# Optimization experiments

Measured on AMD Instinct MI355X. Metric: run time of the kernel, lower is better.

## Reference

```python
import jax, jax.numpy as jnp
import numpy as np

N_NODES = 50000
N_EDGES = 800000
N_GRAPHS = 512
F_IN = 96
HID = 128


def gcn_conv(x, src, dst, W, b, n_nodes):
    # PyG GCNConv: add self-loops, symmetric normalization, scatter-add aggregation.
    h = x @ W  # [N, H] transform first (cheaper than per-edge transform)
    # in-degree from edges (weight 1) plus the self-loop
    deg = jax.ops.segment_sum(jnp.ones_like(dst, dtype=h.dtype), dst,
                              num_segments=n_nodes) + 1.0  # [N]
    dinv = jax.lax.rsqrt(deg)  # D^{-1/2}
    norm = dinv[src] * dinv[dst]  # [E] edge norm
    msg = h[src] * norm[:, None]  # [E, H] gather + scale
    agg = jax.ops.segment_sum(msg, dst, num_segments=n_nodes)  # scatter-add
    agg = agg + h * (1.0 / deg)[:, None]  # self-loop contribution (norm = 1/deg)
    return agg + b


def global_mean_pool(x, batch, num_graphs):
    sums = jax.ops.segment_sum(x, batch, num_segments=num_graphs)  # [G, H]
    cnt = jax.ops.segment_sum(jnp.ones((x.shape[0],), x.dtype), batch,
                              num_segments=num_graphs)  # [G]
    return sums / jnp.maximum(cnt, 1.0)[:, None]


def setup_inputs() -> dict:
    key = jax.random.key(0)
    ks = jax.random.split(key, 8)
    x = jax.random.normal(ks[0], (N_NODES, F_IN), dtype=jnp.float32)
    edge_index = jax.random.randint(ks[1], (2, N_EDGES), 0, N_NODES, dtype=jnp.int64)
    batch = jnp.sort(jax.random.randint(ks[2], (N_NODES,), 0, N_GRAPHS, dtype=jnp.int64))
    W1 = jax.random.normal(ks[3], (F_IN, HID), dtype=jnp.float32) * (1.0 / np.sqrt(F_IN))
    b1 = jnp.zeros((HID,), jnp.float32)
    W2 = jax.random.normal(ks[4], (HID, HID), dtype=jnp.float32) * (1.0 / np.sqrt(HID))
    b2 = jnp.zeros((HID,), jnp.float32)
    Wlin = jax.random.normal(ks[5], (HID, 2), dtype=jnp.float32) * (1.0 / np.sqrt(HID))
    blin = jnp.zeros((2,), jnp.float32)
    return {"x": x, "edge_index": edge_index, "batch": batch, "num_graphs": N_GRAPHS,
            "W1": W1, "b1": b1, "W2": W2, "b2": b2, "Wlin": Wlin, "blin": blin}


def reference(x, edge_index, batch, num_graphs, W1, b1, W2, b2, Wlin, blin):
    src, dst = edge_index[0], edge_index[1]
    n = x.shape[0]
    h = jax.nn.relu(gcn_conv(x, src, dst, W1, b1, n))
    h = jax.nn.relu(gcn_conv(h, src, dst, W2, b2, n))
    g = global_mean_pool(h, batch, num_graphs)  # [G, H]
    # dropout(p=0.2) is identity in eval mode
    return g @ Wlin + blin  # [G, 2]
```

## Files before the change

### kernel.cpp

```cpp
#include <hip/hip_runtime.h>

#define N_NODES 50000
#define N_PAD   50048
#define N_EDGES 800000
#define N_GRAPHS 512
#define F_IN 96
#define HID 128
#define NBUCK 196
#define CHUNK 4096
#define NCH   196
#define NB_G 782

typedef __bf16 bf16x8 __attribute__((ext_vector_type(8)));
typedef float  f32x4  __attribute__((ext_vector_type(4)));

__device__ __forceinline__ unsigned short f2bf(float f) {
    union { float f; unsigned u; } v; v.f = f;
    unsigned r = v.u + 0x7FFFu + ((v.u >> 16) & 1u);
    return (unsigned short)(r >> 16);
}
__device__ __forceinline__ float bflo(unsigned u) {
    union { unsigned u; float f; } v; v.u = u << 16; return v.f;
}
__device__ __forceinline__ float bfhi(unsigned u) {
    union { unsigned u; float f; } v; v.u = u & 0xFFFF0000u; return v.f;
}

__device__ __forceinline__ uint4 frag_of(const float* __restrict__ W, int KS, int idx) {
    int t = idx / (KS * 64);
    int rem = idx % (KS * 64);
    int s = rem / 64;
    int l = rem & 63;
    int n = t * 16 + (l & 15);
    int k0 = s * 32 + (l >> 4) * 8;
    unsigned short v[8];
#pragma unroll
    for (int j = 0; j < 8; ++j) v[j] = f2bf(W[(long)(k0 + j) * 128 + n]);
    uint4 o;
    o.x = (unsigned)v[0] | ((unsigned)v[1] << 16);
    o.y = (unsigned)v[2] | ((unsigned)v[3] << 16);
    o.z = (unsigned)v[4] | ((unsigned)v[5] << 16);
    o.w = (unsigned)v[6] | ((unsigned)v[7] << 16);
    return o;
}

__global__ __launch_bounds__(256) void k1_fused(const int* __restrict__ dst,
                                                const float* __restrict__ W1,
                                                const float* __restrict__ W2,
                                                unsigned short* __restrict__ W2f,
                                                int* __restrict__ bh,
                                                const float* __restrict__ x,
                                                unsigned short* __restrict__ hp) {
    __shared__ uint4 w1lds[1536];
    int blk = blockIdx.x;
    int tid = threadIdx.x;

    if (blk < NB_G) {
        for (int idx = tid; idx < 1536; idx += 256) w1lds[idx] = frag_of(W1, 3, idx);
        __syncthreads();

        const int KS = 3;
        const int wave = tid >> 6, lane = tid & 63;
        const int r0 = blk * 64 + wave * 16;
        f32x4 acc[8];
#pragma unroll
        for (int t = 0; t < 8; ++t) acc[t] = (f32x4){0.f, 0.f, 0.f, 0.f};
        int arow = r0 + (lane & 15);
        if (arow >= N_NODES) arow = N_NODES - 1;
        const int kq = (lane >> 4) * 8;
        for (int s = 0; s < KS; ++s) {
            const float* ap = x + (long)arow * F_IN + s * 32 + kq;
            float4 a0 = *(const float4*)(ap);
            float4 a1 = *(const float4*)(ap + 4);
            union { uint4 u; bf16x8 b; } af;
            af.u.x = (unsigned)f2bf(a0.x) | ((unsigned)f2bf(a0.y) << 16);
            af.u.y = (unsigned)f2bf(a0.z) | ((unsigned)f2bf(a0.w) << 16);
            af.u.z = (unsigned)f2bf(a1.x) | ((unsigned)f2bf(a1.y) << 16);
            af.u.w = (unsigned)f2bf(a1.z) | ((unsigned)f2bf(a1.w) << 16);
#pragma unroll
            for (int t = 0; t < 8; ++t) {
                union { uint4 u; bf16x8 b; } bfr;
                bfr.u = w1lds[(t * KS + s) * 64 + lane];
                acc[t] = __builtin_amdgcn_mfma_f32_16x16x32_bf16(af.b, bfr.b, acc[t], 0, 0, 0);
            }
        }
        const int q = lane >> 4;
#pragma unroll
        for (int t = 0; t < 8; ++t) {
            int col = t * 16 + (lane & 15);
#pragma unroll
            for (int r = 0; r < 4; ++r) {
                int row = r0 + q * 4 + r;
                if (row < N_NODES) hp[(long)row * 128 + col] = f2bf(acc[t][r]);
            }
        }
    } else if (blk < NB_G + NCH) {
        int* bhist = (int*)w1lds;
        int c = blk - NB_G;
        for (int i = tid; i < NBUCK; i += 256) bhist[i] = 0;
        __syncthreads();
        int e0 = c * CHUNK, e1 = min(e0 + CHUNK, N_EDGES);
        int n4 = (e1 - e0) >> 2;
        const uint4* d4 = (const uint4*)(dst + e0);
        for (int i = tid; i < n4; i += 256) {
            uint4 d = d4[i];
            atomicAdd(&bhist[d.x >> 8], 1);
            atomicAdd(&bhist[d.y >> 8], 1);
            atomicAdd(&bhist[d.z >> 8], 1);
            atomicAdd(&bhist[d.w >> 8], 1);
        }
        __syncthreads();
        for (int i = tid; i < NBUCK; i += 256) bh[c * NBUCK + i] = bhist[i];
    } else {
        int idx = (blk - NB_G - NCH) * 256 + tid;
        *(uint4*)(W2f + (long)idx * 8) = frag_of(W2, 4, idx);
    }
}

__global__ __launch_bounds__(256) void goff_scan(const int* __restrict__ bh,
                                                 int* __restrict__ goff,
                                                 int* __restrict__ total) {
    __shared__ int s[256];
    int b = blockIdx.x;
    int c = threadIdx.x;
    int v = (c < NCH) ? bh[c * NBUCK + b] : 0;
    s[c] = v;
    __syncthreads();
#pragma unroll
    for (int off = 1; off < 256; off <<= 1) {
        int t = 0;
        if (c >= off) t = s[c - off];
        __syncthreads();
        if (c >= off) s[c] += t;
        __syncthreads();
    }
    if (c < NCH) goff[c * NBUCK + b] = s[c] - v;
    if (c == 255) total[b] = s[255];
}

__global__ __launch_bounds__(256) void scatter_pairs(const int* __restrict__ src,
                                                     const int* __restrict__ dst,
                                                     const int* __restrict__ goff,
                                                     const int* __restrict__ total,
                                                     unsigned* __restrict__ ebuf) {
    __shared__ int ts[256];
    __shared__ int lgoff[NBUCK];
    __shared__ int lcur[NBUCK];
    int tid = threadIdx.x;
    int c = blockIdx.x;
    int tv = (tid < NBUCK) ? total[tid] : 0;
    ts[tid] = tv;
    __syncthreads();
#pragma unroll
    for (int off = 1; off < 256; off <<= 1) {
        int t = 0;
        if (tid >= off) t = ts[tid - off];
        __syncthreads();
        if (tid >= off) ts[tid] += t;
        __syncthreads();
    }
    if (tid < NBUCK) {
        lgoff[tid] = goff[c * NBUCK + tid] + (ts[tid] - tv);
        lcur[tid] = 0;
    }
    __syncthreads();
    int e0 = c * CHUNK, e1 = min(e0 + CHUNK, N_EDGES);
    for (int e = e0 + tid; e < e1; e += 256) {
        int d = dst[e];
        int b = d >> 8;
        int slot = atomicAdd(&lcur[b], 1);
        ebuf[lgoff[b] + slot] = (unsigned)src[e] | ((unsigned)(d & 255) << 16);
    }
}

__global__ __launch_bounds__(256) void bucket_sort(const unsigned* __restrict__ ebuf,
                                                   const int* __restrict__ total,
                                                   int* __restrict__ rowstart,
                                                   int* __restrict__ cnt,
                                                   float* __restrict__ dinv,
                                                   int* __restrict__ esrc) {
    __shared__ int ts[256];
    __shared__ int lcnt[256];
    __shared__ int ssc[256];
    __shared__ int ncur[256];
    int b = blockIdx.x, tid = threadIdx.x;
    int tv = (tid < NBUCK) ? total[tid] : 0;
    ts[tid] = tv;
    __syncthreads();
#pragma unroll
    for (int off = 1; off < 256; off <<= 1) {
        int t = 0;
        if (tid >= off) t = ts[tid - off];
        __syncthreads();
        if (tid >= off) ts[tid] += t;
        __syncthreads();
    }
    int r1 = ts[b];
    int r0 = r1 - total[b];
    int nbase = b * 256;
    lcnt[tid] = 0;
    __syncthreads();
    for (int i = r0 + tid; i < r1; i += 256)
        atomicAdd(&lcnt[ebuf[i] >> 16], 1);
    __syncthreads();
    int c = lcnt[tid];
    ssc[tid] = c;
    __syncthreads();
#pragma unroll
    for (int off = 1; off < 256; off <<= 1) {
        int t = 0;
        if (tid >= off) t = ssc[tid - off];
        __syncthreads();
        if (tid >= off) ssc[tid] += t;
        __syncthreads();
    }
    int rs = r0 + ssc[tid] - c;
    ncur[tid] = rs;
    int node = nbase + tid;
    if (node < N_NODES) {
        rowstart[node] = rs;
        cnt[node] = c;
        dinv[node] = rsqrtf((float)c + 1.0f);
    }
    __syncthreads();
    for (int i = r0 + tid; i < r1; i += 256) {
        unsigned p = ebuf[i];
        int pos = atomicAdd(&ncur[p >> 16], 1);
        esrc[pos] = (int)(p & 0xFFFFu);
    }
}

__global__ __launch_bounds__(256) void aggregate_w(const uint4* __restrict__ hp4,
                                                   const int* __restrict__ esrc,
                                                   const int* __restrict__ rowstart,
                                                   const int* __restrict__ cnt,
                                                   const float* __restrict__ dinv,
                                                   const float* __restrict__ bias,
                                                   uint4* __restrict__ hout4) {
    int node = blockIdx.x * 4 + (threadIdx.x >> 6);
    if (node >= N_NODES) return;
    int lane = threadIdx.x & 63;
    int eslot = lane >> 4;
    int ug = lane & 15;
    int start = rowstart[node];
    int end = start + cnt[node];

    float a[8];
#pragma unroll
    for (int k = 0; k < 8; ++k) a[k] = 0.f;

    for (int j = start; j < end; j += 16) {
        int e[4];
        uint4 v[4];
        float w[4];
#pragma unroll
        for (int q = 0; q < 4; ++q) {
            e[q] = j + q * 4 + eslot;
            int s = esrc[min(e[q], end - 1)];
            v[q] = hp4[(long)s * 16 + ug];
            w[q] = dinv[s];
        }
#pragma unroll
        for (int q = 0; q < 4; ++q) {
            if (e[q] < end) {
                a[0] += w[q] * bflo(v[q].x); a[1] += w[q] * bfhi(v[q].x);
                a[2] += w[q] * bflo(v[q].y); a[3] += w[q] * bfhi(v[q].y);
                a[4] += w[q] * bflo(v[q].z); a[5] += w[q] * bfhi(v[q].z);
                a[6] += w[q] * bflo(v[q].w); a[7] += w[q] * bfhi(v[q].w);
            }
        }
    }

#pragma unroll
    for (int k = 0; k < 8; ++k) {
        a[k] += __shfl_xor(a[k], 16);
        a[k] += __shfl_xor(a[k], 32);
    }

    if (eslot == 0) {
        float d = dinv[node];
        uint4 vs = hp4[(long)node * 16 + ug];
        a[0] += d * bflo(vs.x); a[1] += d * bfhi(vs.x);
        a[2] += d * bflo(vs.y); a[3] += d * bfhi(vs.y);
        a[4] += d * bflo(vs.z); a[5] += d * bfhi(vs.z);
        a[6] += d * bflo(vs.w); a[7] += d * bfhi(vs.w);
        float4 b0 = *(const float4*)(bias + ug * 8);
        float4 b1 = *(const float4*)(bias + ug * 8 + 4);
        float o0 = fmaxf(d * a[0] + b0.x, 0.f), o1 = fmaxf(d * a[1] + b0.y, 0.f);
        float o2 = fmaxf(d * a[2] + b0.z, 0.f), o3 = fmaxf(d * a[3] + b0.w, 0.f);
        float o4 = fmaxf(d * a[4] + b1.x, 0.f), o5 = fmaxf(d * a[5] + b1.y, 0.f);
        float o6 = fmaxf(d * a[6] + b1.z, 0.f), o7 = fmaxf(d * a[7] + b1.w, 0.f);
        uint4 o;
        o.x = (unsigned)f2bf(o0) | ((unsigned)f2bf(o1) << 16);
        o.y = (unsigned)f2bf(o2) | ((unsigned)f2bf(o3) << 16);
        o.z = (unsigned)f2bf(o4) | ((unsigned)f2bf(o5) << 16);
        o.w = (unsigned)f2bf(o6) | ((unsigned)f2bf(o7) << 16);
        hout4[(long)node * 16 + ug] = o;
    }
}

__global__ __launch_bounds__(256) void gemm_mfma_bf16A(const unsigned short* __restrict__ A,
                                                       const unsigned short* __restrict__ Wf,
                                                       const float* __restrict__ dinv,
                                                       unsigned short* __restrict__ hp) {
    const int KS = 4;
    const int wave = threadIdx.x >> 6;
    const int lane = threadIdx.x & 63;
    const int r0 = blockIdx.x * 64 + wave * 16;

    f32x4 acc[8];
#pragma unroll
    for (int t = 0; t < 8; ++t) acc[t] = (f32x4){0.f, 0.f, 0.f, 0.f};

    const int arow = r0 + (lane & 15);
    const int kq = (lane >> 4) * 8;

    for (int s = 0; s < KS; ++s) {
        union { uint4 u; bf16x8 b; } af;
        af.u = *(const uint4*)(A + (long)arow * HID + s * 32 + kq);
#pragma unroll
        for (int t = 0; t < 8; ++t) {
            union { uint4 u; bf16x8 b; } bfr;
            bfr.u = *(const uint4*)(Wf + ((long)(t * KS + s) * 64 + lane) * 8);
            acc[t] = __builtin_amdgcn_mfma_f32_16x16x32_bf16(af.b, bfr.b, acc[t], 0, 0, 0);
        }
    }

    const int q = lane >> 4;
    float dv[4];
#pragma unroll
    for (int r = 0; r < 4; ++r) {
        int row = r0 + q * 4 + r;
        dv[r] = dinv[row < N_NODES ? row : 0];
    }
#pragma unroll
    for (int t = 0; t < 8; ++t) {
        int col = t * 16 + (lane & 15);
#pragma unroll
        for (int r = 0; r < 4; ++r) {
            int row = r0 + q * 4 + r;
            if (row < N_NODES)
                hp[(long)row * 128 + col] = f2bf(acc[t][r] * dv[r]);
        }
    }
}

__global__ __launch_bounds__(256) void aggregate4(const uint4* __restrict__ hp4,
                                                  const int* __restrict__ esrc,
                                                  const int* __restrict__ rowstart,
                                                  const int* __restrict__ cnt,
                                                  const float* __restrict__ dinv,
                                                  const float* __restrict__ bias,
                                                  uint4* __restrict__ hout4) {
    int node = blockIdx.x * 4 + (threadIdx.x >> 6);
    if (node >= N_NODES) return;
    int lane = threadIdx.x & 63;
    int eslot = lane >> 4;
    int ug = lane & 15;
    int start = rowstart[node];
    int end = start + cnt[node];

    float a[8];
#pragma unroll
    for (int k = 0; k < 8; ++k) a[k] = 0.f;

    for (int j = start; j < end; j += 16) {
        int e[4];
        uint4 v[4];
#pragma unroll
        for (int q = 0; q < 4; ++q) {
            e[q] = j + q * 4 + eslot;
            int s = esrc[min(e[q], end - 1)];
            v[q] = hp4[(long)s * 16 + ug];
        }
#pragma unroll
        for (int q = 0; q < 4; ++q) {
            if (e[q] < end) {
                a[0] += bflo(v[q].x); a[1] += bfhi(v[q].x);
                a[2] += bflo(v[q].y); a[3] += bfhi(v[q].y);
                a[4] += bflo(v[q].z); a[5] += bfhi(v[q].z);
                a[6] += bflo(v[q].w); a[7] += bfhi(v[q].w);
            }
        }
    }

#pragma unroll
    for (int k = 0; k < 8; ++k) {
        a[k] += __shfl_xor(a[k], 16);
        a[k] += __shfl_xor(a[k], 32);
    }

    if (eslot == 0) {
        uint4 vs = hp4[(long)node * 16 + ug];
        a[0] += bflo(vs.x); a[1] += bfhi(vs.x);
        a[2] += bflo(vs.y); a[3] += bfhi(vs.y);
        a[4] += bflo(vs.z); a[5] += bfhi(vs.z);
        a[6] += bflo(vs.w); a[7] += bfhi(vs.w);
        float d = dinv[node];
        float4 b0 = *(const float4*)(bias + ug * 8);
        float4 b1 = *(const float4*)(bias + ug * 8 + 4);
        float o0 = fmaxf(d * a[0] + b0.x, 0.f), o1 = fmaxf(d * a[1] + b0.y, 0.f);
        float o2 = fmaxf(d * a[2] + b0.z, 0.f), o3 = fmaxf(d * a[3] + b0.w, 0.f);
        float o4 = fmaxf(d * a[4] + b1.x, 0.f), o5 = fmaxf(d * a[5] + b1.y, 0.f);
        float o6 = fmaxf(d * a[6] + b1.z, 0.f), o7 = fmaxf(d * a[7] + b1.w, 0.f);
        uint4 o;
        o.x = (unsigned)f2bf(o0) | ((unsigned)f2bf(o1) << 16);
        o.y = (unsigned)f2bf(o2) | ((unsigned)f2bf(o3) << 16);
        o.z = (unsigned)f2bf(o4) | ((unsigned)f2bf(o5) << 16);
        o.w = (unsigned)f2bf(o6) | ((unsigned)f2bf(o7) << 16);
        hout4[(long)node * 16 + ug] = o;
    }
}

__global__ __launch_bounds__(128) void pool_head(const unsigned short* __restrict__ h,
                                                 const int* __restrict__ batch,
                                                 const float* __restrict__ Wlin,
                                                 const float* __restrict__ blin,
                                                 float* __restrict__ out) {
    __shared__ int bnd[2];
    int g = blockIdx.x;
    int c = threadIdx.x;
    if (c < 2) {
        int target = g + c;
        int lo = 0, hi = N_NODES;
        while (lo < hi) {
            int mid = (lo + hi) >> 1;
            if (batch[mid] < target) lo = mid + 1;
            else hi = mid;
        }
        bnd[c] = lo;
    }
    __syncthreads();
    int s = bnd[0], e = bnd[1];

    float sum = 0.f;
    for (int i = s; i < e; ++i) {
        union { unsigned u; float f; } v;
        v.u = (unsigned)h[(long)i * 128 + c] << 16;
        sum += v.f;
    }
    float inv = (e > s) ? 1.0f / (float)(e - s) : 1.0f;
    float m = sum * inv;

    __shared__ float red[128][2];
    red[c][0] = m * Wlin[c * 2 + 0];
    red[c][1] = m * Wlin[c * 2 + 1];
    __syncthreads();
#pragma unroll
    for (int off = 64; off > 0; off >>= 1) {
        if (c < off) {
            red[c][0] += red[c + off][0];
            red[c][1] += red[c + off][1];
        }
        __syncthreads();
    }
    if (c < 2) out[g * 2 + c] = red[0][c] + blin[c];
}

extern "C" void kernel_launch(void* const* d_in, const int* in_sizes, int n_in,
                              void* d_out, int out_size, void* d_ws, size_t ws_size,
                              hipStream_t stream) {
    const float* x    = (const float*)d_in[0];
    const int*   ei   = (const int*)d_in[1];
    const int*   batch= (const int*)d_in[2];
    const float* W1   = (const float*)d_in[4];
    const float* b1   = (const float*)d_in[5];
    const float* W2   = (const float*)d_in[6];
    const float* b2   = (const float*)d_in[7];
    const float* Wlin = (const float*)d_in[8];
    const float* blin = (const float*)d_in[9];
    float* out = (float*)d_out;

    const int* src = ei;
    const int* dst = ei + N_EDGES;

    char* ws = (char*)d_ws;
    const size_t KB = 1024;
    const size_t MB = 1048576;

    float*    dinv     = (float*)(ws);
    int*      cnt      = (int*)  (ws + 256 * KB);
    int*      rowstart = (int*)  (ws + 512 * KB);
    int*      total    = (int*)  (ws + 768 * KB);
    int*      bh       = (int*)  (ws + 832 * KB);
    int*      goff     = (int*)  (ws + 1 * MB);
    unsigned* ebuf     = (unsigned*)(ws + 2 * MB);
    int*      esrc     = (int*)  (ws + 9 * MB);
    unsigned short* W2f = (unsigned short*)(ws + 12 * MB + 576 * KB);
    unsigned short* hp  = (unsigned short*)(ws + 13 * MB);
    unsigned short* h   = (unsigned short*)(ws + 26 * MB);

    const int NB_AG = (N_NODES + 3) / 4;

    k1_fused<<<NB_G + NCH + 8, 256, 0, stream>>>(dst, W1, W2, W2f, bh, x, hp);
    goff_scan<<<NBUCK, 256, 0, stream>>>(bh, goff, total);
    scatter_pairs<<<NCH, 256, 0, stream>>>(src, dst, goff, total, ebuf);
    bucket_sort<<<NBUCK, 256, 0, stream>>>(ebuf, total, rowstart, cnt, dinv, esrc);

    aggregate_w<<<NB_AG, 256, 0, stream>>>((const uint4*)hp, esrc, rowstart, cnt, dinv, b1, (uint4*)h);

    gemm_mfma_bf16A<<<NB_G, 256, 0, stream>>>(h, W2f, dinv, hp);
    aggregate4<<<NB_AG, 256, 0, stream>>>((const uint4*)hp, esrc, rowstart, cnt, dinv, b2, (uint4*)h);

    pool_head<<<N_GRAPHS, 128, 0, stream>>>(h, batch, Wlin, blin, out);
}
```

Baseline: 241.6 us.

## Fuse layer-1 aggregation with layer-2 GEMM through shared memory

Merges the first-layer neighbor aggregation kernel and the second-layer MFMA GEMM into one kernel. Each block aggregates 16 nodes, stages the bf16 rows in padded LDS, then each wave computes two 16-column output tiles. This removes one launch and the global write and re-read of the intermediate hidden features. In exchange, each block has more serial work per wave (4 nodes each), uses a new output buffer, and the tail nodes rely on 50000 dividing evenly by 16.

```diff
diff --git a/kernel.cpp b/kernel.cpp
--- a/kernel.cpp
+++ b/kernel.cpp
@@ -230,117 +230,108 @@
     }
 }
 
-__global__ __launch_bounds__(256) void aggregate_w(const uint4* __restrict__ hp4,
-                                                   const int* __restrict__ esrc,
-                                                   const int* __restrict__ rowstart,
-                                                   const int* __restrict__ cnt,
-                                                   const float* __restrict__ dinv,
-                                                   const float* __restrict__ bias,
-                                                   uint4* __restrict__ hout4) {
-    int node = blockIdx.x * 4 + (threadIdx.x >> 6);
-    if (node >= N_NODES) return;
-    int lane = threadIdx.x & 63;
-    int eslot = lane >> 4;
-    int ug = lane & 15;
-    int start = rowstart[node];
-    int end = start + cnt[node];
-
-    float a[8];
-#pragma unroll
-    for (int k = 0; k < 8; ++k) a[k] = 0.f;
-
-    for (int j = start; j < end; j += 16) {
-        int e[4];
-        uint4 v[4];
-        float w[4];
-#pragma unroll
-        for (int q = 0; q < 4; ++q) {
-            e[q] = j + q * 4 + eslot;
-            int s = esrc[min(e[q], end - 1)];
-            v[q] = hp4[(long)s * 16 + ug];
-            w[q] = dinv[s];
-        }
-#pragma unroll
-        for (int q = 0; q < 4; ++q) {
-            if (e[q] < end) {
-                a[0] += w[q] * bflo(v[q].x); a[1] += w[q] * bfhi(v[q].x);
-                a[2] += w[q] * bflo(v[q].y); a[3] += w[q] * bfhi(v[q].y);
-                a[4] += w[q] * bflo(v[q].z); a[5] += w[q] * bfhi(v[q].z);
-                a[6] += w[q] * bflo(v[q].w); a[7] += w[q] * bfhi(v[q].w);
+#define H1_STRIDE 17
+__global__ __launch_bounds__(256) void agg1_gemm2(const uint4* __restrict__ hp4,
+                                                  const int* __restrict__ esrc,
+                                                  const int* __restrict__ rowstart,
+                                                  const int* __restrict__ cnt,
+                                                  const float* __restrict__ dinv,
+                                                  const float* __restrict__ b1,
+                                                  const unsigned short* __restrict__ W2f,
+                                                  unsigned short* __restrict__ hp2) {
+    __shared__ uint4 h1[16 * H1_STRIDE];
+    const int tid = threadIdx.x;
+    const int wave = tid >> 6, lane = tid & 63;
+    const int eslot = lane >> 4, ug = lane & 15;
+    const int nbase = blockIdx.x * 16;
+
+    for (int i = 0; i < 4; ++i) {
+        int node = nbase + wave * 4 + i;
+        int start = rowstart[node];
+        int end = start + cnt[node];
+
+        float a[8];
+#pragma unroll
+        for (int k = 0; k < 8; ++k) a[k] = 0.f;
+
+        for (int j = start; j < end; j += 16) {
+            int e[4];
+            uint4 v[4];
+            float w[4];
+#pragma unroll
+            for (int q = 0; q < 4; ++q) {
+                e[q] = j + q * 4 + eslot;
+                int s = esrc[min(e[q], end - 1)];
+                v[q] = hp4[(long)s * 16 + ug];
+                w[q] = dinv[s];
             }
-        }
-    }
-
-#pragma unroll
-    for (int k = 0; k < 8; ++k) {
-        a[k] += __shfl_xor(a[k], 16);
-        a[k] += __shfl_xor(a[k], 32);
-    }
-
-    if (eslot == 0) {
-        float d = dinv[node];
-        uint4 vs = hp4[(long)node * 16 + ug];
-        a[0] += d * bflo(vs.x); a[1] += d * bfhi(vs.x);
-        a[2] += d * bflo(vs.y); a[3] += d * bfhi(vs.y);
-        a[4] += d * bflo(vs.z); a[5] += d * bfhi(vs.z);
-        a[6] += d * bflo(vs.w); a[7] += d * bfhi(vs.w);
-        float4 b0 = *(const float4*)(bias + ug * 8);
-        float4 b1 = *(const float4*)(bias + ug * 8 + 4);
-        float o0 = fmaxf(d * a[0] + b0.x, 0.f), o1 = fmaxf(d * a[1] + b0.y, 0.f);
-        float o2 = fmaxf(d * a[2] + b0.z, 0.f), o3 = fmaxf(d * a[3] + b0.w, 0.f);
-        float o4 = fmaxf(d * a[4] + b1.x, 0.f), o5 = fmaxf(d * a[5] + b1.y, 0.f);
-        float o6 = fmaxf(d * a[6] + b1.z, 0.f), o7 = fmaxf(d * a[7] + b1.w, 0.f);
-        uint4 o;
-        o.x = (unsigned)f2bf(o0) | ((unsigned)f2bf(o1) << 16);
-        o.y = (unsigned)f2bf(o2) | ((unsigned)f2bf(o3) << 16);
-        o.z = (unsigned)f2bf(o4) | ((unsigned)f2bf(o5) << 16);
-        o.w = (unsigned)f2bf(o6) | ((unsigned)f2bf(o7) << 16);
-        hout4[(long)node * 16 + ug] = o;
-    }
-}
-
-__global__ __launch_bounds__(256) void gemm_mfma_bf16A(const unsigned short* __restrict__ A,
-                                                       const unsigned short* __restrict__ Wf,
-                                                       const float* __restrict__ dinv,
-                                                       unsigned short* __restrict__ hp) {
+#pragma unroll
+            for (int q = 0; q < 4; ++q) {
+                if (e[q] < end) {
+                    a[0] += w[q] * bflo(v[q].x); a[1] += w[q] * bfhi(v[q].x);
+                    a[2] += w[q] * bflo(v[q].y); a[3] += w[q] * bfhi(v[q].y);
+                    a[4] += w[q] * bflo(v[q].z); a[5] += w[q] * bfhi(v[q].z);
+                    a[6] += w[q] * bflo(v[q].w); a[7] += w[q] * bfhi(v[q].w);
+                }
+            }
+        }
+
+#pragma unroll
+        for (int k = 0; k < 8; ++k) {
+            a[k] += __shfl_xor(a[k], 16);
+            a[k] += __shfl_xor(a[k], 32);
+        }
+
+        if (eslot == 0) {
+            float d = dinv[node];
+            uint4 vs = hp4[(long)node * 16 + ug];
+            a[0] += d * bflo(vs.x); a[1] += d * bfhi(vs.x);
+            a[2] += d * bflo(vs.y); a[3] += d * bfhi(vs.y);
+            a[4] += d * bflo(vs.z); a[5] += d * bfhi(vs.z);
+            a[6] += d * bflo(vs.w); a[7] += d * bfhi(vs.w);
+            float4 c0 = *(const float4*)(b1 + ug * 8);
+            float4 c1 = *(const float4*)(b1 + ug * 8 + 4);
+            float o0 = fmaxf(d * a[0] + c0.x, 0.f), o1 = fmaxf(d * a[1] + c0.y, 0.f);
+            float o2 = fmaxf(d * a[2] + c0.z, 0.f), o3 = fmaxf(d * a[3] + c0.w, 0.f);
+            float o4 = fmaxf(d * a[4] + c1.x, 0.f), o5 = fmaxf(d * a[5] + c1.y, 0.f);
+            float o6 = fmaxf(d * a[6] + c1.z, 0.f), o7 = fmaxf(d * a[7] + c1.w, 0.f);
+            uint4 o;
+            o.x = (unsigned)f2bf(o0) | ((unsigned)f2bf(o1) << 16);
+            o.y = (unsigned)f2bf(o2) | ((unsigned)f2bf(o3) << 16);
+            o.z = (unsigned)f2bf(o4) | ((unsigned)f2bf(o5) << 16);
+            o.w = (unsigned)f2bf(o6) | ((unsigned)f2bf(o7) << 16);
+            h1[(wave * 4 + i) * H1_STRIDE + ug] = o;
+        }
+    }
+    __syncthreads();
+
     const int KS = 4;
-    const int wave = threadIdx.x >> 6;
-    const int lane = threadIdx.x & 63;
-    const int r0 = blockIdx.x * 64 + wave * 16;
-
-    f32x4 acc[8];
-#pragma unroll
-    for (int t = 0; t < 8; ++t) acc[t] = (f32x4){0.f, 0.f, 0.f, 0.f};
-
-    const int arow = r0 + (lane & 15);
-    const int kq = (lane >> 4) * 8;
-
+    f32x4 acc[2];
+    acc[0] = (f32x4){0.f, 0.f, 0.f, 0.f};
+    acc[1] = (f32x4){0.f, 0.f, 0.f, 0.f};
+    const int m = lane & 15;
     for (int s = 0; s < KS; ++s) {
         union { uint4 u; bf16x8 b; } af;
-        af.u = *(const uint4*)(A + (long)arow * HID + s * 32 + kq);
-#pragma unroll
-        for (int t = 0; t < 8; ++t) {
+        af.u = h1[m * H1_STRIDE + s * 4 + eslot];
+#pragma unroll
+        for (int tt = 0; tt < 2; ++tt) {
+            int t = wave * 2 + tt;
             union { uint4 u; bf16x8 b; } bfr;
-            bfr.u = *(const uint4*)(Wf + ((long)(t * KS + s) * 64 + lane) * 8);
-            acc[t] = __builtin_amdgcn_mfma_f32_16x16x32_bf16(af.b, bfr.b, acc[t], 0, 0, 0);
-        }
-    }
-
+            bfr.u = *(const uint4*)(W2f + ((long)(t * KS + s) * 64 + lane) * 8);
+            acc[tt] = __builtin_amdgcn_mfma_f32_16x16x32_bf16(af.b, bfr.b, acc[tt], 0, 0, 0);
+        }
+    }
     const int q = lane >> 4;
     float dv[4];
 #pragma unroll
-    for (int r = 0; r < 4; ++r) {
-        int row = r0 + q * 4 + r;
-        dv[r] = dinv[row < N_NODES ? row : 0];
-    }
-#pragma unroll
-    for (int t = 0; t < 8; ++t) {
-        int col = t * 16 + (lane & 15);
+    for (int r = 0; r < 4; ++r) dv[r] = dinv[nbase + q * 4 + r];
+#pragma unroll
+    for (int tt = 0; tt < 2; ++tt) {
+        int col = (wave * 2 + tt) * 16 + (lane & 15);
 #pragma unroll
         for (int r = 0; r < 4; ++r) {
-            int row = r0 + q * 4 + r;
-            if (row < N_NODES)
-                hp[(long)row * 128 + col] = f2bf(acc[t][r] * dv[r]);
+            int row = nbase + q * 4 + r;
+            hp2[(long)row * 128 + col] = f2bf(acc[tt][r] * dv[r]);
         }
     }
 }
@@ -488,19 +479,20 @@
     int*      esrc     = (int*)  (ws + 9 * MB);
     unsigned short* W2f = (unsigned short*)(ws + 12 * MB + 576 * KB);
     unsigned short* hp  = (unsigned short*)(ws + 13 * MB);
-    unsigned short* h   = (unsigned short*)(ws + 26 * MB);
+    unsigned short* hp2 = (unsigned short*)(ws + 26 * MB);
+    unsigned short* h   = (unsigned short*)(ws + 39 * MB);
 
     const int NB_AG = (N_NODES + 3) / 4;
+    const int NB_F  = N_NODES / 16;
 
     k1_fused<<<NB_G + NCH + 8, 256, 0, stream>>>(dst, W1, W2, W2f, bh, x, hp);
     goff_scan<<<NBUCK, 256, 0, stream>>>(bh, goff, total);
     scatter_pairs<<<NCH, 256, 0, stream>>>(src, dst, goff, total, ebuf);
     bucket_sort<<<NBUCK, 256, 0, stream>>>(ebuf, total, rowstart, cnt, dinv, esrc);
 
-    aggregate_w<<<NB_AG, 256, 0, stream>>>((const uint4*)hp, esrc, rowstart, cnt, dinv, b1, (uint4*)h);
-
-    gemm_mfma_bf16A<<<NB_G, 256, 0, stream>>>(h, W2f, dinv, hp);
-    aggregate4<<<NB_AG, 256, 0, stream>>>((const uint4*)hp, esrc, rowstart, cnt, dinv, b2, (uint4*)h);
+    agg1_gemm2<<<NB_F, 256, 0, stream>>>((const uint4*)hp, esrc, rowstart, cnt, dinv, b1, W2f, hp2);
+
+    aggregate4<<<NB_AG, 256, 0, stream>>>((const uint4*)hp2, esrc, rowstart, cnt, dinv, b2, (uint4*)h);
 
     pool_head<<<N_GRAPHS, 128, 0, stream>>>(h, batch, Wlin, blin, out);
 }
```

Result: faster. 232.4 us (-3.8%).
